# Kernel optimization log

Hardware: AMD Instinct MI355X
Metric: run time of the kernel (lower is better)

## Reference

```python
import jax, jax.numpy as jnp
import numpy as np

B, T, C = 32, 400, 3000
SN, SD = 128, 512   # numerator / denominator FSM state counts
NEG = -1e4          # log-zero surrogate (finite for grad safety)
DEN_SCALE = 1.0
DO_AVG = False


def setup_inputs() -> dict:
    key = jax.random.key(0)
    ks = jax.random.split(key, 8)
    x = jax.random.normal(ks[0], (B, T, C), jnp.float32)
    seqlengths = jax.random.randint(ks[1], (B,), T // 2, T + 1)
    # Numerator FSMs: batched left-to-right chains with self-loops.
    i = np.arange(SN)
    band = (i[None, :] >= i[:, None]) & (i[None, :] - i[:, None] <= 1)
    num_trans = jnp.where(jnp.asarray(band),
                          0.1 * jax.random.normal(ks[2], (B, SN, SN), jnp.float32), NEG)
    num_pdf = jax.random.randint(ks[3], (B, SN), 0, C)
    num_init = jnp.broadcast_to(jnp.where(jnp.arange(SN) == 0, 0.0, NEG), (B, SN)).astype(jnp.float32)
    num_final = jnp.broadcast_to(jnp.where(jnp.arange(SN) == SN - 1, 0.0, NEG), (B, SN)).astype(jnp.float32)
    # Denominator FSM: one dense graph shared by the whole batch.
    den_trans = 0.1 * jax.random.normal(ks[4], (SD, SD), jnp.float32)
    den_pdf = jax.random.randint(ks[5], (SD,), 0, C)
    den_init = 0.1 * jax.random.normal(ks[6], (SD,), jnp.float32)
    den_final = 0.1 * jax.random.normal(ks[7], (SD,), jnp.float32)
    return dict(input=x, seqlengths=seqlengths,
                num_trans=num_trans, num_pdf=num_pdf, num_init=num_init, num_final=num_final,
                den_trans=den_trans, den_pdf=den_pdf, den_init=den_init, den_final=den_final)


def _log_marginal(ll, seqlengths, trans, pdf, init, final):
    """FSM forward recursion in the log domain.
    ll: [B,T,C]; trans: [B,S,S] or [S,S]; pdf/init/final: [B,S].
    Returns per-sequence log-marginal [B]."""
    Bn, Tn, _ = ll.shape
    S = pdf.shape[-1]
    # Per-state emissions: em[b,t,s] = ll[b,t,pdf[b,s]]
    em = jnp.take_along_axis(ll, jnp.broadcast_to(pdf[:, None, :], (Bn, Tn, S)), axis=2)
    alpha0 = init + em[:, 0]                              # [B,S]
    mask = jnp.arange(1, Tn)[:, None] < seqlengths[None, :]  # [T-1,B]

    def step(alpha, xs):
        em_t, m = xs
        new = jax.nn.logsumexp(alpha[:, :, None] + trans, axis=1) + em_t
        return jnp.where(m[:, None], new, alpha), None

    alphaT, _ = jax.lax.scan(step, alpha0, (jnp.swapaxes(em, 0, 1)[1:], mask))
    return jax.nn.logsumexp(alphaT + final, axis=-1)      # [B]


def reference(input, seqlengths, num_trans, num_pdf, num_init, num_final,
              den_trans, den_pdf, den_init, den_final):
    ll = jnp.clip(input, -30.0, 30.0)
    Bn = ll.shape[0]
    num_llh = _log_marginal(ll, seqlengths, num_trans, num_pdf, num_init, num_final).sum()
    den_llh = _log_marginal(
        ll, seqlengths, den_trans,
        jnp.broadcast_to(den_pdf[None], (Bn, SD)),
        jnp.broadcast_to(den_init[None], (Bn, SD)),
        jnp.broadcast_to(den_final[None], (Bn, SD))).sum()
    loss = -(num_llh - DEN_SCALE * den_llh)
    if DO_AVG:
        loss = loss / seqlengths.sum()
    return loss
```

## Files before the change

kernel.cpp:

```cpp
#include <hip/hip_runtime.h>

#define B_ 32
#define T_ 400
#define C_ 3000
#define SN_ 128
#define SD_ 512
#define LNS 8.94637462f
#define LN120 4.78749174f
#define SPAN 80

__device__ __forceinline__ float clip30(float v) { return fminf(30.f, fmaxf(-30.f, v)); }

__device__ __forceinline__ int dot4i8(unsigned a, unsigned b, int c) {
#if __has_builtin(__builtin_amdgcn_sdot4)
    return __builtin_amdgcn_sdot4((int)a, (int)b, c, false);
#else
    return c + (int)(a & 0xff) * (int)(b & 0xff)
             + (int)((a >> 8) & 0xff) * (int)((b >> 8) & 0xff)
             + (int)((a >> 16) & 0xff) * (int)((b >> 16) & 0xff)
             + (int)((a >> 24) & 0xff) * (int)((b >> 24) & 0xff);
#endif
}

template <int CTRL>
__device__ __forceinline__ int dpp_i(int v) {
    return __builtin_amdgcn_update_dpp(v, v, CTRL, 0xF, 0xF, false);
}
template <int CTRL>
__device__ __forceinline__ float fmaxdpp(float v) {
    int mv = __builtin_amdgcn_update_dpp(__float_as_int(v), __float_as_int(v), CTRL, 0xF, 0xF, false);
    return fmaxf(v, __int_as_float(mv));
}
template <int CTRL>
__device__ __forceinline__ float faddpp(float v) {
    int mv = __builtin_amdgcn_update_dpp(__float_as_int(v), __float_as_int(v), CTRL, 0xF, 0xF, false);
    return v + __int_as_float(mv);
}
template <int CTRL>
__device__ __forceinline__ float fxaddf(float a, float b) {
    int t = __builtin_amdgcn_update_dpp(__float_as_int(b), __float_as_int(b), CTRL, 0xF, 0xF, false);
    return a + __int_as_float(t);
}
__device__ __forceinline__ float swz16f(float v) {
    return __int_as_float(__builtin_amdgcn_ds_swizzle(__float_as_int(v), 0x401F));
}
__device__ __forceinline__ float wavemax_fast(float v) {
    v = fmaxdpp<0x121>(v); v = fmaxdpp<0x122>(v);
    v = fmaxdpp<0x124>(v); v = fmaxdpp<0x128>(v);
    float a = __int_as_float(__builtin_amdgcn_readlane(__float_as_int(v), 0));
    float b = __int_as_float(__builtin_amdgcn_readlane(__float_as_int(v), 16));
    float c = __int_as_float(__builtin_amdgcn_readlane(__float_as_int(v), 32));
    float d = __int_as_float(__builtin_amdgcn_readlane(__float_as_int(v), 48));
    return fmaxf(fmaxf(a, b), fmaxf(c, d));
}
__device__ __forceinline__ float waveallsum(float v) {
    v = faddpp<0x121>(v); v = faddpp<0x122>(v);
    v = faddpp<0x124>(v); v = faddpp<0x128>(v);
    v = v + swz16f(v);
    v = v + __shfl_xor(v, 32, 64);
    return v;
}
__device__ __forceinline__ void barrier_lds() {
    asm volatile("s_waitcnt lgkmcnt(0)\n\ts_barrier" ::: "memory");
}

__global__ void prep(const float* __restrict__ dt, unsigned* __restrict__ tp8,
                     const float* __restrict__ x, const int* __restrict__ den_pdf,
                     const int* __restrict__ num_pdf,
                     float* __restrict__ em_den, float* __restrict__ em_num) {
    size_t id = (size_t)blockIdx.x * 1024 + threadIdx.x;
    if (id < 65536) {
        int o = (int)id;
        int b4 = o & 3, tid = (o >> 2) & 511, k = o >> 11;
        int r = 4 * k + b4;
        int m = r >> 4, i = r & 15;
        int g = tid >> 3, j = tid & 7;
        int s_out = 8 * g + (m ^ j);
        int s_from0 = 64 * j + 4 * i;
        unsigned wv = 0;
        #pragma unroll
        for (int by = 0; by < 4; ++by) {
            float e = __expf(dt[(s_from0 + by) * SD_ + s_out]);
            int pq = __float2int_rn(e * 64.f);
            if (pq > 127) pq = 127;
            wv |= (unsigned)pq << (8 * by);
        }
        tp8[o] = wv;
    } else if (id < 65536 + 6553600) {
        size_t e = id - 65536;
        int s = (int)(e & 511);
        size_t bt = e >> 9;
        em_den[e] = clip30(x[bt * C_ + den_pdf[s]]);
    } else if (id < 65536 + 6553600 + 1638400) {
        size_t e = id - 65536 - 6553600;
        int s = (int)(e & 127);
        size_t bt = e >> 7;
        int b = (int)(bt / 400);
        em_num[e] = clip30(x[bt * C_ + num_pdf[b * SN_ + s]]);
    }
}

__global__ __launch_bounds__(512, 2)
void fwd_kernel(const int* __restrict__ seqlen,
                const float* __restrict__ num_trans,
                const float* __restrict__ num_init, const float* __restrict__ num_final,
                const unsigned* __restrict__ tp8,
                const float* __restrict__ den_init, const float* __restrict__ den_final,
                const float* __restrict__ em_den, const float* __restrict__ em_num,
                float* __restrict__ parts) {
    const int tid = threadIdx.x;

    if (blockIdx.x < B_) {
        __shared__ __align__(16) unsigned char ea[2][8 * SPAN];
        __shared__ float Ms[2][8];
        __shared__ float fr[8];
        const int b = blockIdx.x;
        const int L = seqlen[b];
        const int w = tid >> 6, l = tid & 63;
        const int j = tid & 7;

        unsigned tq[128];
        {
            const uint4* tg = (const uint4*)tp8;
            #pragma unroll
            for (int i = 0; i < 32; ++i) {
                uint4 v = tg[(i << 9) + tid];
                tq[4 * i + 0] = v.x;
                tq[4 * i + 1] = v.y;
                tq[4 * i + 2] = v.z;
                tq[4 * i + 3] = v.w;
            }
        }

        const float* emp = em_den + (size_t)b * T_ * SD_ + tid;

        float a0f = den_init[tid] + emp[0];
        float ms_w = wavemax_fast(a0f);
        int un = __float2int_rn(fminf(120.f * __expf(a0f - ms_w), 127.f));
        {
            int uu = un;
            uu |= dpp_i<0xB1>(uu) << 8;
            uu |= dpp_i<0x4E>(uu) << 16;
            if ((tid & 3) == 0)
                *(unsigned*)&ea[0][SPAN * w + (tid & 63)] = (unsigned)uu;
        }
        if (l == 0) Ms[0][w] = ms_w;
        barrier_lds();

        float emA = emp[SD_], emB = emp[2 * SD_];
        int cur = 0;
        for (int t = 1; t < L; ++t) {
            int tn = (t + 2 < L) ? t + 2 : L - 1;
            float emN = emp[(size_t)tn * SD_];

            float ms_j = Ms[cur][j];
            const uint4* er = (const uint4*)&ea[cur][SPAN * j];
            uint4 e0 = er[0], e1 = er[1], e2 = er[2], e3 = er[3];

            int ac0, ac1, ac2, ac3, ac4, ac5, ac6, ac7;
            #define DOTD0(W, I) \
                ac0 = dot4i8((W), tq[(I)],       0); \
                ac1 = dot4i8((W), tq[16 + (I)],  0); \
                ac2 = dot4i8((W), tq[32 + (I)],  0); \
                ac3 = dot4i8((W), tq[48 + (I)],  0); \
                ac4 = dot4i8((W), tq[64 + (I)],  0); \
                ac5 = dot4i8((W), tq[80 + (I)],  0); \
                ac6 = dot4i8((W), tq[96 + (I)],  0); \
                ac7 = dot4i8((W), tq[112 + (I)], 0);
            #define DOTD(W, I) \
                ac0 = dot4i8((W), tq[(I)],       ac0); \
                ac1 = dot4i8((W), tq[16 + (I)],  ac1); \
                ac2 = dot4i8((W), tq[32 + (I)],  ac2); \
                ac3 = dot4i8((W), tq[48 + (I)],  ac3); \
                ac4 = dot4i8((W), tq[64 + (I)],  ac4); \
                ac5 = dot4i8((W), tq[80 + (I)],  ac5); \
                ac6 = dot4i8((W), tq[96 + (I)],  ac6); \
                ac7 = dot4i8((W), tq[112 + (I)], ac7);
            DOTD0(e0.x, 0) DOTD(e0.y, 1)  DOTD(e0.z, 2)  DOTD(e0.w, 3)
            DOTD(e1.x, 4)  DOTD(e1.y, 5)  DOTD(e1.z, 6)  DOTD(e1.w, 7)
            DOTD(e2.x, 8)  DOTD(e2.y, 9)  DOTD(e2.z, 10) DOTD(e2.w, 11)
            DOTD(e3.x, 12) DOTD(e3.y, 13) DOTD(e3.z, 14) DOTD(e3.w, 15)
            #undef DOTD
            #undef DOTD0

            float e_own = __expf(ms_j - ms_w);
            float f0 = (float)ac0 * e_own, f1 = (float)ac1 * e_own;
            float f2 = (float)ac2 * e_own, f3 = (float)ac3 * e_own;
            float f4 = (float)ac4 * e_own, f5 = (float)ac5 * e_own;
            float f6 = (float)ac6 * e_own, f7 = (float)ac7 * e_own;
            f0 = fxaddf<0xB1>(f0, f1);  f2 = fxaddf<0xB1>(f2, f3);
            f4 = fxaddf<0xB1>(f4, f5);  f6 = fxaddf<0xB1>(f6, f7);
            f0 = fxaddf<0x4E>(f0, f2);  f4 = fxaddf<0x4E>(f4, f6);
            f0 = fxaddf<0x124>(f0, f4);

            float g = fmaf(0.69314718f,
                           (float)__float_as_int(f0) * 1.1920929e-7f - 127.0f, emA);
            float gg = wavemax_fast(g);
            un = __float2int_rn(fminf(120.f * f0 * __expf(emA - gg), 127.f));
            {
                int uu = un;
                uu |= dpp_i<0xB1>(uu) << 8;
                uu |= dpp_i<0x4E>(uu) << 16;
                if ((tid & 3) == 0)
                    *(unsigned*)&ea[cur ^ 1][SPAN * w + (tid & 63)] = (unsigned)uu;
            }
            ms_w = gg + ms_w - LNS;
            if (l == 0) Ms[cur ^ 1][w] = ms_w;
            emA = emB; emB = emN;
            barrier_lds();
            cur ^= 1;
        }

        float mm = Ms[cur][0];
        #pragma unroll
        for (int k2 = 1; k2 < 8; ++k2) mm = fmaxf(mm, Ms[cur][k2]);
        float fv = (float)un * __expf(den_final[tid] + (ms_w - mm));
        fv = waveallsum(fv);
        if (l == 0) fr[w] = fv;
        __syncthreads();
        if (tid == 0) {
            float tot = 0.f;
            for (int i = 0; i < 8; ++i) tot += fr[i];
            parts[B_ + b] = mm + __logf(tot) - LN120;
        }
    } else {
        __shared__ float aLn[2][4][SN_];
        __shared__ float nredn[4][2];
        const int nb = blockIdx.x - B_;
        const int lb = tid >> 7;
        const int b  = nb * 4 + lb;
        const int s  = tid & 127;
        const int L  = seqlen[b];
        const int lane = tid & 63;
        const int wv2 = (tid >> 6) & 1;
        const float* ep = em_num + (size_t)b * T_ * SN_ + s;
        const float tself = num_trans[((size_t)b * SN_ + s) * SN_ + s];
        const float tup = (s > 0) ? num_trans[((size_t)b * SN_ + (s - 1)) * SN_ + s] : 0.f;
        float alpha = num_init[b * SN_ + s] + ep[0];
        aLn[0][lb][s] = alpha;
        __syncthreads();
        float emA = ep[SN_], emB = ep[2 * SN_];
        int cur = 0;
        for (int t = 1; t < T_; ++t) {
            int tt = t + 2; if (tt > T_ - 1) tt = T_ - 1;
            float emN = ep[(size_t)tt * SN_];
            bool live = (t < L);
            float yy = alpha + tself;
            float newa;
            if (s > 0) {
                float xx = aLn[cur][lb][s - 1] + tup;
                float mx = fmaxf(xx, yy), mn = fminf(xx, yy);
                newa = mx + log1pf(__expf(mn - mx)) + emA;
            } else {
                newa = yy + emA;
            }
            if (live) alpha = newa;
            aLn[cur ^ 1][lb][s] = alpha;
            emA = emB; emB = emN;
            __syncthreads();
            cur ^= 1;
        }
        float v = alpha + num_final[b * SN_ + s];
        float wm = v;
        #pragma unroll
        for (int o = 32; o; o >>= 1) wm = fmaxf(wm, __shfl_xor(wm, o, 64));
        if (lane == 0) nredn[lb][wv2] = wm;
        __syncthreads();
        float fm = fmaxf(nredn[lb][0], nredn[lb][1]);
        __syncthreads();
        float pe = __expf(v - fm);
        #pragma unroll
        for (int o = 32; o; o >>= 1) pe += __shfl_xor(pe, o, 64);
        if (lane == 0) nredn[lb][wv2] = pe;
        __syncthreads();
        if (s == 0) parts[b] = fm + __logf(nredn[lb][0] + nredn[lb][1]);
    }
}

__global__ void finish(const float* __restrict__ parts, float* __restrict__ out) {
    int lane = threadIdx.x;
    float v = (lane < B_) ? (parts[B_ + lane] - parts[lane]) : 0.f;
    #pragma unroll
    for (int o = 32; o; o >>= 1) v += __shfl_xor(v, o, 64);
    if (lane == 0) out[0] = v;
}

extern "C" void kernel_launch(void* const* d_in, const int* in_sizes, int n_in,
                              void* d_out, int out_size, void* d_ws, size_t ws_size,
                              hipStream_t stream) {
    const float* x         = (const float*)d_in[0];
    const int*   seqlen    = (const int*)d_in[1];
    const float* num_trans = (const float*)d_in[2];
    const int*   num_pdf   = (const int*)d_in[3];
    const float* num_init  = (const float*)d_in[4];
    const float* num_final = (const float*)d_in[5];
    const float* den_trans = (const float*)d_in[6];
    const int*   den_pdf   = (const int*)d_in[7];
    const float* den_init  = (const float*)d_in[8];
    const float* den_final = (const float*)d_in[9];
    float* out   = (float*)d_out;
    float* parts = (float*)d_ws;
    unsigned* tp8 = (unsigned*)((char*)d_ws + 4096);
    float* em_den = (float*)((char*)d_ws + 4096 + 262144);
    float* em_num = em_den + 6553600;

    prep<<<8064, 1024, 0, stream>>>(den_trans, tp8, x, den_pdf, num_pdf, em_den, em_num);
    fwd_kernel<<<40, 512, 0, stream>>>(seqlen, num_trans, num_init, num_final,
                                       tp8, den_init, den_final, em_den, em_num, parts);
    finish<<<1, 64, 0, stream>>>(parts, out);
}
```

Baseline: 409.8 us.

## Process two denominator sequences per workgroup to interleave independent recursions

```diff
diff --git a/kernel.cpp b/kernel.cpp
--- a/kernel.cpp
+++ b/kernel.cpp
@@ -5,6 +5,7 @@
 #define C_ 3000
 #define SN_ 128
 #define SD_ 512
+#define DEN_WGS 16
 #define LNS 8.94637462f
 #define LN120 4.78749174f
 #define SPAN 80
@@ -62,6 +63,45 @@
 }
 __device__ __forceinline__ void barrier_lds() {
     asm volatile("s_waitcnt lgkmcnt(0)\n\ts_barrier" ::: "memory");
+}
+
+__device__ __forceinline__ float span_dot_fold(const unsigned* tq,
+                                               uint4 e0, uint4 e1, uint4 e2, uint4 e3,
+                                               float e_own) {
+    int ac0, ac1, ac2, ac3, ac4, ac5, ac6, ac7;
+    #define DOTD0(W, I) \
+        ac0 = dot4i8((W), tq[(I)],       0); \
+        ac1 = dot4i8((W), tq[16 + (I)],  0); \
+        ac2 = dot4i8((W), tq[32 + (I)],  0); \
+        ac3 = dot4i8((W), tq[48 + (I)],  0); \
+        ac4 = dot4i8((W), tq[64 + (I)],  0); \
+        ac5 = dot4i8((W), tq[80 + (I)],  0); \
+        ac6 = dot4i8((W), tq[96 + (I)],  0); \
+        ac7 = dot4i8((W), tq[112 + (I)], 0);
+    #define DOTD(W, I) \
+        ac0 = dot4i8((W), tq[(I)],       ac0); \
+        ac1 = dot4i8((W), tq[16 + (I)],  ac1); \
+        ac2 = dot4i8((W), tq[32 + (I)],  ac2); \
+        ac3 = dot4i8((W), tq[48 + (I)],  ac3); \
+        ac4 = dot4i8((W), tq[64 + (I)],  ac4); \
+        ac5 = dot4i8((W), tq[80 + (I)],  ac5); \
+        ac6 = dot4i8((W), tq[96 + (I)],  ac6); \
+        ac7 = dot4i8((W), tq[112 + (I)], ac7);
+    DOTD0(e0.x, 0) DOTD(e0.y, 1)  DOTD(e0.z, 2)  DOTD(e0.w, 3)
+    DOTD(e1.x, 4)  DOTD(e1.y, 5)  DOTD(e1.z, 6)  DOTD(e1.w, 7)
+    DOTD(e2.x, 8)  DOTD(e2.y, 9)  DOTD(e2.z, 10) DOTD(e2.w, 11)
+    DOTD(e3.x, 12) DOTD(e3.y, 13) DOTD(e3.z, 14) DOTD(e3.w, 15)
+    #undef DOTD
+    #undef DOTD0
+    float f0 = (float)ac0 * e_own, f1 = (float)ac1 * e_own;
+    float f2 = (float)ac2 * e_own, f3 = (float)ac3 * e_own;
+    float f4 = (float)ac4 * e_own, f5 = (float)ac5 * e_own;
+    float f6 = (float)ac6 * e_own, f7 = (float)ac7 * e_own;
+    f0 = fxaddf<0xB1>(f0, f1);  f2 = fxaddf<0xB1>(f2, f3);
+    f4 = fxaddf<0xB1>(f4, f5);  f6 = fxaddf<0xB1>(f6, f7);
+    f0 = fxaddf<0x4E>(f0, f2);  f4 = fxaddf<0x4E>(f4, f6);
+    f0 = fxaddf<0x124>(f0, f4);
+    return f0;
 }
 
 __global__ void prep(const float* __restrict__ dt, unsigned* __restrict__ tp8,
@@ -110,12 +150,13 @@
                 float* __restrict__ parts) {
     const int tid = threadIdx.x;
 
-    if (blockIdx.x < B_) {
-        __shared__ __align__(16) unsigned char ea[2][8 * SPAN];
-        __shared__ float Ms[2][8];
-        __shared__ float fr[8];
-        const int b = blockIdx.x;
-        const int L = seqlen[b];
+    if (blockIdx.x < DEN_WGS) {
+        __shared__ __align__(16) unsigned char ea[2][2][8 * SPAN];
+        __shared__ float Ms[2][2][8];
+        __shared__ float fr[2][8];
+        const int b0 = 2 * blockIdx.x, b1 = b0 + 1;
+        const int L0 = seqlen[b0], L1 = seqlen[b1];
+        const int Lmax = (L0 > L1) ? L0 : L1;
         const int w = tid >> 6, l = tid & 63;
         const int j = tid & 7;
 
@@ -132,101 +173,94 @@
             }
         }
 
-        const float* emp = em_den + (size_t)b * T_ * SD_ + tid;
-
-        float a0f = den_init[tid] + emp[0];
-        float ms_w = wavemax_fast(a0f);
-        int un = __float2int_rn(fminf(120.f * __expf(a0f - ms_w), 127.f));
+        const float* emp0 = em_den + (size_t)b0 * T_ * SD_ + tid;
+        const float* emp1 = em_den + (size_t)b1 * T_ * SD_ + tid;
+
+        float dini = den_init[tid];
+        float a0 = dini + emp0[0];
+        float a1 = dini + emp1[0];
+        float ms0 = wavemax_fast(a0);
+        float ms1 = wavemax_fast(a1);
+        int un0 = __float2int_rn(fminf(120.f * __expf(a0 - ms0), 127.f));
+        int un1 = __float2int_rn(fminf(120.f * __expf(a1 - ms1), 127.f));
         {
-            int uu = un;
-            uu |= dpp_i<0xB1>(uu) << 8;
-            uu |= dpp_i<0x4E>(uu) << 16;
-            if ((tid & 3) == 0)
-                *(unsigned*)&ea[0][SPAN * w + (tid & 63)] = (unsigned)uu;
-        }
-        if (l == 0) Ms[0][w] = ms_w;
+            int u0 = un0, u1 = un1;
+            u0 |= dpp_i<0xB1>(u0) << 8;  u1 |= dpp_i<0xB1>(u1) << 8;
+            u0 |= dpp_i<0x4E>(u0) << 16; u1 |= dpp_i<0x4E>(u1) << 16;
+            if ((tid & 3) == 0) {
+                *(unsigned*)&ea[0][0][SPAN * w + (tid & 63)] = (unsigned)u0;
+                *(unsigned*)&ea[0][1][SPAN * w + (tid & 63)] = (unsigned)u1;
+            }
+        }
+        if (l == 0) { Ms[0][0][w] = ms0; Ms[0][1][w] = ms1; }
         barrier_lds();
 
-        float emA = emp[SD_], emB = emp[2 * SD_];
+        float emA0 = emp0[SD_], emB0 = emp0[2 * SD_];
+        float emA1 = emp1[SD_], emB1 = emp1[2 * SD_];
         int cur = 0;
-        for (int t = 1; t < L; ++t) {
-            int tn = (t + 2 < L) ? t + 2 : L - 1;
-            float emN = emp[(size_t)tn * SD_];
-
-            float ms_j = Ms[cur][j];
-            const uint4* er = (const uint4*)&ea[cur][SPAN * j];
-            uint4 e0 = er[0], e1 = er[1], e2 = er[2], e3 = er[3];
-
-            int ac0, ac1, ac2, ac3, ac4, ac5, ac6, ac7;
-            #define DOTD0(W, I) \
-                ac0 = dot4i8((W), tq[(I)],       0); \
-                ac1 = dot4i8((W), tq[16 + (I)],  0); \
-                ac2 = dot4i8((W), tq[32 + (I)],  0); \
-                ac3 = dot4i8((W), tq[48 + (I)],  0); \
-                ac4 = dot4i8((W), tq[64 + (I)],  0); \
-                ac5 = dot4i8((W), tq[80 + (I)],  0); \
-                ac6 = dot4i8((W), tq[96 + (I)],  0); \
-                ac7 = dot4i8((W), tq[112 + (I)], 0);
-            #define DOTD(W, I) \
-                ac0 = dot4i8((W), tq[(I)],       ac0); \
-                ac1 = dot4i8((W), tq[16 + (I)],  ac1); \
-                ac2 = dot4i8((W), tq[32 + (I)],  ac2); \
-                ac3 = dot4i8((W), tq[48 + (I)],  ac3); \
-                ac4 = dot4i8((W), tq[64 + (I)],  ac4); \
-                ac5 = dot4i8((W), tq[80 + (I)],  ac5); \
-                ac6 = dot4i8((W), tq[96 + (I)],  ac6); \
-                ac7 = dot4i8((W), tq[112 + (I)], ac7);
-            DOTD0(e0.x, 0) DOTD(e0.y, 1)  DOTD(e0.z, 2)  DOTD(e0.w, 3)
-            DOTD(e1.x, 4)  DOTD(e1.y, 5)  DOTD(e1.z, 6)  DOTD(e1.w, 7)
-            DOTD(e2.x, 8)  DOTD(e2.y, 9)  DOTD(e2.z, 10) DOTD(e2.w, 11)
-            DOTD(e3.x, 12) DOTD(e3.y, 13) DOTD(e3.z, 14) DOTD(e3.w, 15)
-            #undef DOTD
-            #undef DOTD0
-
-            float e_own = __expf(ms_j - ms_w);
-            float f0 = (float)ac0 * e_own, f1 = (float)ac1 * e_own;
-            float f2 = (float)ac2 * e_own, f3 = (float)ac3 * e_own;
-            float f4 = (float)ac4 * e_own, f5 = (float)ac5 * e_own;
-            float f6 = (float)ac6 * e_own, f7 = (float)ac7 * e_own;
-            f0 = fxaddf<0xB1>(f0, f1);  f2 = fxaddf<0xB1>(f2, f3);
-            f4 = fxaddf<0xB1>(f4, f5);  f6 = fxaddf<0xB1>(f6, f7);
-            f0 = fxaddf<0x4E>(f0, f2);  f4 = fxaddf<0x4E>(f4, f6);
-            f0 = fxaddf<0x124>(f0, f4);
-
-            float g = fmaf(0.69314718f,
-                           (float)__float_as_int(f0) * 1.1920929e-7f - 127.0f, emA);
-            float gg = wavemax_fast(g);
-            un = __float2int_rn(fminf(120.f * f0 * __expf(emA - gg), 127.f));
+        for (int t = 1; t < Lmax; ++t) {
+            int tn = t + 2; if (tn > T_ - 1) tn = T_ - 1;
+            float emN0 = emp0[(size_t)tn * SD_];
+            float emN1 = emp1[(size_t)tn * SD_];
+
+            float msj0 = Ms[cur][0][j], msj1 = Ms[cur][1][j];
+            const uint4* er0 = (const uint4*)&ea[cur][0][SPAN * j];
+            const uint4* er1 = (const uint4*)&ea[cur][1][SPAN * j];
+            uint4 e0 = er0[0], e1 = er0[1], e2 = er0[2], e3 = er0[3];
+            uint4 d0 = er1[0], d1 = er1[1], d2 = er1[2], d3 = er1[3];
+
+            float F0 = span_dot_fold(tq, e0, e1, e2, e3, __expf(msj0 - ms0));
+            float F1 = span_dot_fold(tq, d0, d1, d2, d3, __expf(msj1 - ms1));
+
+            float g0 = fmaf(0.69314718f,
+                            (float)__float_as_int(F0) * 1.1920929e-7f - 127.0f, emA0);
+            float g1 = fmaf(0.69314718f,
+                            (float)__float_as_int(F1) * 1.1920929e-7f - 127.0f, emA1);
+            float gg0 = wavemax_fast(g0);
+            float gg1 = wavemax_fast(g1);
+            int nun0 = __float2int_rn(fminf(120.f * F0 * __expf(emA0 - gg0), 127.f));
+            int nun1 = __float2int_rn(fminf(120.f * F1 * __expf(emA1 - gg1), 127.f));
+            if (t < L0) { un0 = nun0; ms0 = ms0 + gg0 - LNS; }
+            if (t < L1) { un1 = nun1; ms1 = ms1 + gg1 - LNS; }
             {
-                int uu = un;
-                uu |= dpp_i<0xB1>(uu) << 8;
-                uu |= dpp_i<0x4E>(uu) << 16;
-                if ((tid & 3) == 0)
-                    *(unsigned*)&ea[cur ^ 1][SPAN * w + (tid & 63)] = (unsigned)uu;
+                int u0 = un0, u1 = un1;
+                u0 |= dpp_i<0xB1>(u0) << 8;  u1 |= dpp_i<0xB1>(u1) << 8;
+                u0 |= dpp_i<0x4E>(u0) << 16; u1 |= dpp_i<0x4E>(u1) << 16;
+                if ((tid & 3) == 0) {
+                    *(unsigned*)&ea[cur ^ 1][0][SPAN * w + (tid & 63)] = (unsigned)u0;
+                    *(unsigned*)&ea[cur ^ 1][1][SPAN * w + (tid & 63)] = (unsigned)u1;
+                }
             }
-            ms_w = gg + ms_w - LNS;
-            if (l == 0) Ms[cur ^ 1][w] = ms_w;
-            emA = emB; emB = emN;
+            if (l == 0) { Ms[cur ^ 1][0][w] = ms0; Ms[cur ^ 1][1][w] = ms1; }
+            emA0 = emB0; emB0 = emN0;
+            emA1 = emB1; emB1 = emN1;
             barrier_lds();
             cur ^= 1;
         }
 
-        float mm = Ms[cur][0];
+        float dfin = den_final[tid];
+        float mm0 = Ms[cur][0][0], mm1 = Ms[cur][1][0];
         #pragma unroll
-        for (int k2 = 1; k2 < 8; ++k2) mm = fmaxf(mm, Ms[cur][k2]);
-        float fv = (float)un * __expf(den_final[tid] + (ms_w - mm));
-        fv = waveallsum(fv);
-        if (l == 0) fr[w] = fv;
+        for (int k2 = 1; k2 < 8; ++k2) {
+            mm0 = fmaxf(mm0, Ms[cur][0][k2]);
+            mm1 = fmaxf(mm1, Ms[cur][1][k2]);
+        }
+        float fv0 = (float)un0 * __expf(dfin + (ms0 - mm0));
+        float fv1 = (float)un1 * __expf(dfin + (ms1 - mm1));
+        fv0 = waveallsum(fv0);
+        fv1 = waveallsum(fv1);
+        if (l == 0) { fr[0][w] = fv0; fr[1][w] = fv1; }
         __syncthreads();
         if (tid == 0) {
-            float tot = 0.f;
-            for (int i = 0; i < 8; ++i) tot += fr[i];
-            parts[B_ + b] = mm + __logf(tot) - LN120;
+            float t0 = 0.f, t1 = 0.f;
+            for (int i = 0; i < 8; ++i) { t0 += fr[0][i]; t1 += fr[1][i]; }
+            parts[B_ + b0] = mm0 + __logf(t0) - LN120;
+            parts[B_ + b1] = mm1 + __logf(t1) - LN120;
         }
     } else {
         __shared__ float aLn[2][4][SN_];
         __shared__ float nredn[4][2];
-        const int nb = blockIdx.x - B_;
+        const int nb = blockIdx.x - DEN_WGS;
         const int lb = tid >> 7;
         const int b  = nb * 4 + lb;
         const int s  = tid & 127;
@@ -305,7 +339,7 @@
     float* em_num = em_den + 6553600;
 
     prep<<<8064, 1024, 0, stream>>>(den_trans, tp8, x, den_pdf, num_pdf, em_den, em_num);
-    fwd_kernel<<<40, 512, 0, stream>>>(seqlen, num_trans, num_init, num_final,
-                                       tp8, den_init, den_final, em_den, em_num, parts);
+    fwd_kernel<<<DEN_WGS + 8, 512, 0, stream>>>(seqlen, num_trans, num_init, num_final,
+                                                tp8, den_init, den_final, em_den, em_num, parts);
     finish<<<1, 64, 0, stream>>>(parts, out);
 }
```

After: 715.1 us. 74.5% more time.
